# Optimization experiments

Hardware: AMD Instinct MI355X
Metric: run time of the kernel (lower is better)

Reference implementation:

```python
import jax, jax.numpy as jnp
import numpy as np

B, S, P, G, E = 16, 1024, 32, 64, 512
HD = E // 2          # head_dim = 256
SCALE = HD ** -0.5
LAMBDA_INIT = 0.8 - 0.6 * float(np.exp(-0.3 * 0.0))  # depth=0 -> 0.2
EPS = 1e-5


def setup_inputs() -> dict:
    key = jax.random.key(0)
    ks = jax.random.split(key, 12)
    inp = {
        'query': jax.random.normal(ks[0], (B, S, E), jnp.float32),
        'key': jax.random.normal(ks[1], (B, P, G, E), jnp.float32),
        'mask': jax.random.randint(ks[2], (B, S), 0, 2).astype(bool),
        'Wq': jax.random.normal(ks[3], (E, E), jnp.float32) * (E ** -0.5),
        'Wk': jax.random.normal(ks[4], (E, E), jnp.float32) * (E ** -0.5),
        'Wv': jax.random.normal(ks[5], (E, E), jnp.float32) * (E ** -0.5),
        'Wo': jax.random.normal(ks[6], (E, E), jnp.float32) * (E ** -0.5),
        'lq1': jax.random.normal(ks[7], (HD,), jnp.float32) * 0.1,
        'lk1': jax.random.normal(ks[8], (HD,), jnp.float32) * 0.1,
        'lq2': jax.random.normal(ks[9], (HD,), jnp.float32) * 0.1,
        'lk2': jax.random.normal(ks[10], (HD,), jnp.float32) * 0.1,
        'gamma': jnp.ones((E,), jnp.float32),
    }
    return inp


def reference(query, key, mask, Wq, Wk, Wv, Wo, lq1, lk1, lq2, lk2, gamma):
    b, s, e = query.shape
    _, p, g, _ = key.shape
    L = p * g
    key2d = key.reshape(b, L, e)

    Q = (query @ Wq).reshape(b, s, 2, HD).transpose(0, 2, 1, 3) * SCALE  # [B,2,S,hd]
    K = (key2d @ Wk).reshape(b, L, 2, HD).transpose(0, 2, 1, 3)          # [B,2,L,hd]
    V = key2d @ Wv                                                       # [B,L,E]

    scores = jnp.einsum('bhsd,bhld->bhsl', Q, K)                         # [B,2,S,L]
    # masked_fill(~mask, 0.0) with mask broadcast [B,1,S,1]
    scores = jnp.where(mask[:, None, :, None], scores, 0.0)
    attn = jax.nn.softmax(scores, axis=-1)

    lam1 = jnp.exp(jnp.sum(lq1 * lk1))
    lam2 = jnp.exp(jnp.sum(lq2 * lk2))
    lam = lam1 - lam2 + LAMBDA_INIT

    diff = attn[:, 0] - lam * attn[:, 1]                                 # [B,S,L]
    out2d = jnp.einsum('bsl,ble->bse', diff, V)                          # [B,S,E]

    # RMSNorm over last dim with affine gamma
    rms = out2d * jax.lax.rsqrt(jnp.mean(out2d * out2d, axis=-1, keepdims=True) + EPS)
    rms = rms * gamma
    out = (rms * (1.0 - LAMBDA_INIT)) @ Wo                               # [B,S,E]

    return out, diff.reshape(b, s, p, g)
```

## Files before the change

### kernel.cpp

```cpp
#include <hip/hip_runtime.h>
#include <hip/hip_bf16.h>


typedef short short8 __attribute__((ext_vector_type(8)));
typedef __bf16 bf16x8 __attribute__((ext_vector_type(8)));
typedef float f32x4 __attribute__((ext_vector_type(4)));

#define LDS_BYTES 16384
#define OUT0_ELEMS 8388608L

__global__ void probe_kernel(const void* gamma, const void* mask, int* flags)
{
    if (threadIdx.x == 0) {
        unsigned g = *(const unsigned*)gamma;
        flags[0] = (g == 0x3F800000u) ? 1 : 0;
        flags[1] = 0;
    }
    __syncthreads();
    const unsigned* mi = (const unsigned*)mask;
    int bad = 0;
    for (int i = threadIdx.x; i < 4096; i += blockDim.x)
        if (mi[i] > 1u) bad = 1;
    if (bad) atomicOr(&flags[1], 1);
}

__global__ void convert_mask(const void* __restrict__ mask, int* __restrict__ mi,
                             const int* __restrict__ flags)
{
    int i = blockIdx.x * 256 + threadIdx.x;
    if (flags[1]) mi[i] = ((const unsigned char*)mask)[i] ? 1 : 0;
    else          mi[i] = ((const int*)mask)[i] ? 1 : 0;
}

__device__ __forceinline__ float read_elem(const void* p, int i, int isf32)
{
    return isf32 ? ((const float*)p)[i]
                 : __bfloat162float(((const __hip_bfloat16*)p)[i]);
}

__global__ void convert_gamma(const void* __restrict__ gamma, float* __restrict__ g,
                              const int* __restrict__ flags)
{
    int i = blockIdx.x * 256 + threadIdx.x;
    g[i] = read_elem(gamma, i, flags[0]);
}

__global__ void transpose_w(const void* __restrict__ Wq, const void* __restrict__ Wk,
                            const void* __restrict__ Wv, const void* __restrict__ Wo,
                            __hip_bfloat16* __restrict__ dst, const int* __restrict__ flags)
{
    int which = blockIdx.y;
    const void* s = (which == 0) ? Wq : (which == 1) ? Wk : (which == 2) ? Wv : Wo;
    __hip_bfloat16* d = dst + (long)which * 262144;
    int idx = blockIdx.x * 256 + threadIdx.x;
    int k = idx >> 9, n = idx & 511;
    d[n * 512 + k] = __float2bfloat16(read_elem(s, idx, flags[0]));
}

__global__ void lam_kernel(const void* __restrict__ lq1, const void* __restrict__ lk1,
                           const void* __restrict__ lq2, const void* __restrict__ lk2,
                           float* __restrict__ lamp, const int* __restrict__ flags)
{
    int t = threadIdx.x;
    int f = flags[0];
    float s1 = 0.0f, s2 = 0.0f;
#pragma unroll
    for (int j = 0; j < 4; ++j) {
        int idx = t * 4 + j;
        s1 += read_elem(lq1, idx, f) * read_elem(lk1, idx, f);
        s2 += read_elem(lq2, idx, f) * read_elem(lk2, idx, f);
    }
#pragma unroll
    for (int off = 1; off < 64; off <<= 1) {
        s1 += __shfl_xor(s1, off);
        s2 += __shfl_xor(s2, off);
    }
    if (t == 0) *lamp = __expf(s1) - __expf(s2) + 0.2f;
}

__global__ void zero_lst(float* __restrict__ lst)
{
    lst[blockIdx.x * 256 + threadIdx.x] = 0.0f;
}

__device__ __forceinline__ void stage_u(const void* A, long aoff, int lda, int af32,
                                        const __hip_bfloat16* B, int ldb,
                                        int kt, char* smem, int tid)
{
    if (af32) {
#pragma unroll
        for (int j = 0; j < 2; ++j) {
            int chunk = j * 256 + tid;
            const float* g = (const float*)A + aoff + (long)(chunk >> 2) * lda + kt + (chunk & 3) * 8;
            f32x4 x0 = *(const f32x4*)g;
            f32x4 x1 = *(const f32x4*)(g + 4);
            __hip_bfloat16 tmp[8];
#pragma unroll
            for (int t = 0; t < 4; ++t) tmp[t] = __float2bfloat16(x0[t]);
#pragma unroll
            for (int t = 0; t < 4; ++t) tmp[4 + t] = __float2bfloat16(x1[t]);
            *(short8*)(smem + chunk * 16) = *(const short8*)tmp;
        }
    } else {
#pragma unroll
        for (int j = 0; j < 2; ++j) {
            int chunk = j * 256 + tid;
            const __hip_bfloat16* g = (const __hip_bfloat16*)A + aoff
                                    + (long)(chunk >> 2) * lda + kt + (chunk & 3) * 8;
            __builtin_amdgcn_global_load_lds(
                (__attribute__((address_space(1))) void*)g,
                (__attribute__((address_space(3))) void*)(smem + chunk * 16), 16, 0, 0);
        }
    }
#pragma unroll
    for (int j = 0; j < 2; ++j) {
        int chunk = j * 256 + tid;
        const __hip_bfloat16* g = B + (long)(chunk >> 2) * ldb + kt + (chunk & 3) * 8;
        __builtin_amdgcn_global_load_lds(
            (__attribute__((address_space(1))) void*)g,
            (__attribute__((address_space(3))) void*)(smem + 8192 + chunk * 16), 16, 0, 0);
    }
}

__device__ __forceinline__ void mfma_block(char* smem, int tid, f32x4 (&acc)[4][4])
{
    const int lane = tid & 63, wid = tid >> 6;
    const int wm = wid >> 1, wn = wid & 1;
    const int lm = lane & 15, lq = lane >> 4;
    short8 a[4], b[4];
#pragma unroll
    for (int i = 0; i < 4; ++i)
        a[i] = *(const short8*)(smem + (wm * 64 + i * 16 + lm) * 64 + lq * 16);
#pragma unroll
    for (int i = 0; i < 4; ++i)
        b[i] = *(const short8*)(smem + 8192 + (wn * 64 + i * 16 + lm) * 64 + lq * 16);
#pragma unroll
    for (int i = 0; i < 4; ++i)
#pragma unroll
        for (int j = 0; j < 4; ++j)
            acc[i][j] = __builtin_amdgcn_mfma_f32_16x16x32_bf16(
                __builtin_bit_cast(bf16x8, a[i]),
                __builtin_bit_cast(bf16x8, b[j]),
                acc[i][j], 0, 0, 0);
}

__device__ __forceinline__ void zero_acc(f32x4 (&acc)[4][4])
{
#pragma unroll
    for (int i = 0; i < 4; ++i)
#pragma unroll
        for (int j = 0; j < 4; ++j)
#pragma unroll
            for (int r = 0; r < 4; ++r) acc[i][j][r] = 0.0f;
}

__device__ __forceinline__ void tile_gemm_u(const void* A, long aoff, int lda, int af32,
                                            const __hip_bfloat16* B, int ldb, int K,
                                            char* smem, int tid, f32x4 (&acc)[4][4])
{
    zero_acc(acc);
    for (int kt = 0; kt < K; kt += 32) {
        __syncthreads();
        stage_u(A, aoff, lda, af32, B, ldb, kt, smem, tid);
        __syncthreads();
        mfma_block(smem, tid, acc);
    }
}

template <int MODE, int AF>
__launch_bounds__(256, 4)
__global__ void gemm_u(const void* __restrict__ A,
                       const __hip_bfloat16* __restrict__ B,
                       void* __restrict__ C,
                       int K, int lda, int ldb, int ldc,
                       long sA, long sB, long sC, float scale,
                       const int* __restrict__ flags)
{
    __shared__ __align__(16) char smem[LDS_BYTES];
    const int tid = threadIdx.x;
    const int bn = blockIdx.x, bm = blockIdx.y, bz = blockIdx.z;
    const int af32 = AF ? flags[0] : 0;
    const long aoff = (long)bz * sA + (long)bm * 128 * lda;
    const __hip_bfloat16* Bb = B + (long)bz * sB + (long)bn * 128 * ldb;

    f32x4 acc[4][4];
    tile_gemm_u(A, aoff, lda, af32, Bb, ldb, K, smem, tid, acc);

    const int f32o = (MODE == 3) ? flags[0] : 0;
    const int lane = tid & 63, wid = tid >> 6;
    const int wm = wid >> 1, wn = wid & 1;
    const int lm = lane & 15, lq = lane >> 4;
#pragma unroll
    for (int im = 0; im < 4; ++im)
#pragma unroll
        for (int in = 0; in < 4; ++in)
#pragma unroll
            for (int r = 0; r < 4; ++r) {
                int row = bm * 128 + wm * 64 + im * 16 + lq * 4 + r;
                int col = bn * 128 + wn * 64 + in * 16 + lm;
                float v = acc[im][in][r] * scale;
                if (MODE == 0) {
                    ((__hip_bfloat16*)C)[bz * sC + (long)row * ldc + col] = __float2bfloat16(v);
                } else if (MODE == 2) {
                    ((float*)C)[bz * sC + (long)row * ldc + col] = v;
                } else if (MODE == 3) {
                    long idx = bz * sC + (long)row * ldc + col;
                    if (f32o) ((float*)C)[idx] = v;
                    else      ((__hip_bfloat16*)C)[idx] = __float2bfloat16(v);
                } else {
                    int bb = row >> 11, l = row & 2047;
                    ((__hip_bfloat16*)C)[((long)bb * 512 + col) * 2048 + l] = __float2bfloat16(v);
                }
            }
}

__device__ __forceinline__ void score_epilogue(
    f32x4 (&acc)[4][4], char* smem, int tid,
    int nt, int st, int b, int bl, const int* __restrict__ mask,
    float* __restrict__ lstats, __hip_bfloat16* __restrict__ P, int h)
{
    const int lane = tid & 63, wid = tid >> 6;
    const int wm = wid >> 1, wn = wid & 1;
    const int lm = lane & 15, lq = lane >> 4;
    float esum[4][4];
#pragma unroll
    for (int im = 0; im < 4; ++im)
#pragma unroll
        for (int r = 0; r < 4; ++r) {
            int rl = wm * 64 + im * 16 + lq * 4 + r;
            int s  = st * 128 + rl;
            int mv = mask[b * 1024 + s];
            float es = 0.0f;
#pragma unroll
            for (int in = 0; in < 4; ++in) {
                int col = nt * 128 + wn * 64 + in * 16 + lm;
                float sc = mv ? acc[im][in][r] : 0.0f;
                float e  = __expf(sc);
                P[((long)bl * 1024 + s) * 2048 + col] = __float2bfloat16(e);
                float t = e;
                t += __shfl_xor(t, 1);
                t += __shfl_xor(t, 2);
                t += __shfl_xor(t, 4);
                t += __shfl_xor(t, 8);
                es += t;
            }
            esum[im][r] = es;
        }
    __syncthreads();
    float* red = (float*)smem;
    if (lm == 0) {
#pragma unroll
        for (int im = 0; im < 4; ++im)
#pragma unroll
            for (int r = 0; r < 4; ++r)
                red[wn * 128 + wm * 64 + im * 16 + lq * 4 + r] = esum[im][r];
    }
    __syncthreads();
    if (tid < 128)
        atomicAdd(&lstats[((long)(b * 2 + h)) * 1024 + st * 128 + tid],
                  red[tid] + red[128 + tid]);
}

__launch_bounds__(256, 3)
__global__ void score_kernel(const __hip_bfloat16* __restrict__ Q,
                             const __hip_bfloat16* __restrict__ Km,
                             const int* __restrict__ mask,
                             float* __restrict__ lstats,
                             __hip_bfloat16* __restrict__ P0,
                             __hip_bfloat16* __restrict__ P1,
                             int bbase)
{
    __shared__ __align__(16) char smem[LDS_BYTES];
    const int tid = threadIdx.x;
    const int nt = blockIdx.x, st = blockIdx.y, bl = blockIdx.z;
    const int b = bl + bbase;
    const long A0 = ((long)b * 1024 + st * 128) * 512;
    const __hip_bfloat16* B0 = Km + ((long)b * 2048 + nt * 128) * 512;

    f32x4 acc[4][4];
    tile_gemm_u(Q, A0, 512, 0, B0, 512, 256, smem, tid, acc);
    score_epilogue(acc, smem, tid, nt, st, b, bl, mask, lstats, P0, 0);
    tile_gemm_u(Q, A0 + 256, 512, 0, B0 + 256, 512, 256, smem, tid, acc);
    score_epilogue(acc, smem, tid, nt, st, b, bl, mask, lstats, P1, 1);
}

__launch_bounds__(256, 2)
__global__ void dv_wide(const __hip_bfloat16* __restrict__ P0,
                        const __hip_bfloat16* __restrict__ P1,
                        const __hip_bfloat16* __restrict__ Vt,
                        const float* __restrict__ lst,
                        const float* __restrict__ lamp,
                        float* __restrict__ o2d,
                        void* __restrict__ dout,
                        const int* __restrict__ flags)
{
    __shared__ __align__(16) char smem[36864];
    const int tid = threadIdx.x;
    const int bm = blockIdx.x, b = blockIdx.y;
    const float lam = *lamp;

    const int arow = tid >> 2;
    const int acol = (tid & 3) * 8;
    const int srow = bm * 32 + (arow & 31);
    float i0 = 0.0f, i1 = 0.0f;
    if (tid < 128) {
        i0 = 1.0f / lst[((long)(b * 2)) * 1024 + srow];
        i1 = lam  / lst[((long)(b * 2 + 1)) * 1024 + srow];
    }
    const __hip_bfloat16* Bb = Vt + (long)b * (512L * 2048);
    const int f32o = flags[0];
    float* doutF = (float*)dout + OUT0_ELEMS;
    __hip_bfloat16* doutH = (__hip_bfloat16*)dout + OUT0_ELEMS;

    f32x4 acc[2][8];
#pragma unroll
    for (int im = 0; im < 2; ++im)
#pragma unroll
        for (int in = 0; in < 8; ++in)
#pragma unroll
            for (int r = 0; r < 4; ++r) acc[im][in][r] = 0.0f;

    const int lane = tid & 63, wid = tid >> 6;
    const int lm = lane & 15, lq = lane >> 4;

    for (int kt = 0; kt < 2048; kt += 32) {
        __syncthreads();
#pragma unroll
        for (int j = 0; j < 8; ++j) {
            int chunk = j * 256 + tid;
            const __hip_bfloat16* g = Bb + (long)(chunk >> 2) * 2048 + kt + (chunk & 3) * 8;
            __builtin_amdgcn_global_load_lds(
                (__attribute__((address_space(1))) void*)g,
                (__attribute__((address_space(3))) void*)(smem + 4096 + chunk * 16), 16, 0, 0);
        }
        float d[8];
        union { short8 v; __hip_bfloat16 h[8]; } ta;
        if (tid < 128) {
            long off = ((long)b * 1024 + srow) * 2048 + kt + acol;
            union { short8 v; __hip_bfloat16 h[8]; } u0, u1;
            u0.v = *(const short8*)(P0 + off);
            u1.v = *(const short8*)(P1 + off);
#pragma unroll
            for (int t = 0; t < 8; ++t)
                d[t] = __bfloat162float(u0.h[t]) * i0 - __bfloat162float(u1.h[t]) * i1;
#pragma unroll
            for (int t = 0; t < 8; ++t) ta.h[t] = __float2bfloat16(d[t]);
            *(short8*)(smem + (arow & 31) * 64 + (tid & 3) * 16) = ta.v;
        }
        __syncthreads();
        if (tid < 128) {
            long g = ((long)b * 1024 + srow) * 2048 + kt + acol;
            if (f32o) {
                f32x4 v0, v1;
#pragma unroll
                for (int t = 0; t < 4; ++t) { v0[t] = d[t]; v1[t] = d[4 + t]; }
                *(f32x4*)(doutF + g)     = v0;
                *(f32x4*)(doutF + g + 4) = v1;
            } else {
                *(short8*)(doutH + g) = ta.v;
            }
        }
        short8 af[2], bf[8];
#pragma unroll
        for (int im = 0; im < 2; ++im)
            af[im] = *(const short8*)(smem + (im * 16 + lm) * 64 + lq * 16);
#pragma unroll
        for (int in = 0; in < 8; ++in)
            bf[in] = *(const short8*)(smem + 4096 + (wid * 128 + in * 16 + lm) * 64 + lq * 16);
#pragma unroll
        for (int im = 0; im < 2; ++im)
#pragma unroll
            for (int in = 0; in < 8; ++in)
                acc[im][in] = __builtin_amdgcn_mfma_f32_16x16x32_bf16(
                    __builtin_bit_cast(bf16x8, af[im]),
                    __builtin_bit_cast(bf16x8, bf[in]),
                    acc[im][in], 0, 0, 0);
    }

#pragma unroll
    for (int im = 0; im < 2; ++im)
#pragma unroll
        for (int in = 0; in < 8; ++in)
#pragma unroll
            for (int r = 0; r < 4; ++r) {
                int row = bm * 32 + im * 16 + lq * 4 + r;
                int col = wid * 128 + in * 16 + lm;
                o2d[((long)b * 1024 + row) * 512 + col] = acc[im][in][r];
            }
}

__launch_bounds__(256, 3)
__global__ void dv_fused(const __hip_bfloat16* __restrict__ P0,
                         const __hip_bfloat16* __restrict__ P1,
                         const __hip_bfloat16* __restrict__ Vt,
                         const float* __restrict__ lst,
                         const float* __restrict__ lamp,
                         float* __restrict__ o2d,
                         void* __restrict__ dout,
                         int bbase, const int* __restrict__ flags)
{
    __shared__ __align__(16) char smem[LDS_BYTES];
    const int tid = threadIdx.x;
    const int bn = blockIdx.x, bm = blockIdx.y, bz = blockIdx.z;
    const int b = bz + bbase;
    const float lam = *lamp;

    int srow[2]; float i0[2], i1[2];
#pragma unroll
    for (int j = 0; j < 2; ++j) {
        srow[j] = bm * 128 + j * 64 + (tid >> 2);
        i0[j] = 1.0f / lst[((long)(b * 2)) * 1024 + srow[j]];
        i1[j] = lam  / lst[((long)(b * 2 + 1)) * 1024 + srow[j]];
    }

    const __hip_bfloat16* Bb = Vt + (long)b * (512L * 2048) + (long)bn * 128 * 2048;
    const int f32o = flags[0];
    float* doutF = (float*)dout + OUT0_ELEMS;
    __hip_bfloat16* doutH = (__hip_bfloat16*)dout + OUT0_ELEMS;

    f32x4 acc[4][4];
    zero_acc(acc);

    for (int kt = 0; kt < 2048; kt += 32) {
        __syncthreads();
#pragma unroll
        for (int j = 0; j < 2; ++j) {
            int chunk = j * 256 + tid;
            int kc = kt + (chunk & 3) * 8;
            long off = ((long)bz * 1024 + srow[j]) * 2048 + kc;
            union { short8 v; __hip_bfloat16 h[8]; } u0, u1;
            u0.v = *(const short8*)(P0 + off);
            u1.v = *(const short8*)(P1 + off);
            float d[8];
#pragma unroll
            for (int t = 0; t < 8; ++t)
                d[t] = __bfloat162float(u0.h[t]) * i0[j]
                     - __bfloat162float(u1.h[t]) * i1[j];
            __hip_bfloat16 tmp[8];
#pragma unroll
            for (int t = 0; t < 8; ++t) tmp[t] = __float2bfloat16(d[t]);
            *(short8*)(smem + chunk * 16) = *(const short8*)tmp;
            if (bn == 0) {
                long g = ((long)b * 1024 + srow[j]) * 2048 + kc;
                if (f32o) {
                    f32x4 v0, v1;
#pragma unroll
                    for (int t = 0; t < 4; ++t) { v0[t] = d[t]; v1[t] = d[4 + t]; }
                    *(f32x4*)(doutF + g)     = v0;
                    *(f32x4*)(doutF + g + 4) = v1;
                } else {
                    *(short8*)(doutH + g) = *(const short8*)tmp;
                }
            }
        }
#pragma unroll
        for (int j = 0; j < 2; ++j) {
            int chunk = j * 256 + tid;
            const __hip_bfloat16* g = Bb + (long)(chunk >> 2) * 2048 + kt + (chunk & 3) * 8;
            __builtin_amdgcn_global_load_lds(
                (__attribute__((address_space(1))) void*)g,
                (__attribute__((address_space(3))) void*)(smem + 8192 + chunk * 16), 16, 0, 0);
        }
        __syncthreads();
        mfma_block(smem, tid, acc);
    }

    const int lane = tid & 63, wid = tid >> 6;
    const int wm = wid >> 1, wn = wid & 1;
    const int lm = lane & 15, lq = lane >> 4;
#pragma unroll
    for (int im = 0; im < 4; ++im)
#pragma unroll
        for (int in = 0; in < 4; ++in)
#pragma unroll
            for (int r = 0; r < 4; ++r) {
                int row = bm * 128 + wm * 64 + im * 16 + lq * 4 + r;
                int col = bn * 128 + wn * 64 + in * 16 + lm;
                o2d[((long)b * 1024 + row) * 512 + col] = acc[im][in][r];
            }
}

__global__ void finalize_kernel(__hip_bfloat16* P0,
                                const __hip_bfloat16* __restrict__ P1,
                                const float* __restrict__ lstats,
                                const float* __restrict__ lamp,
                                void* dout, int bbase,
                                const int* __restrict__ flags)
{
    const long row = blockIdx.x;
    const int bl = (int)(row >> 10), s = (int)(row & 1023);
    const int b  = bl + bbase;
    const int tid = threadIdx.x;
    const float lam = *lamp;
    const float i0 = 1.0f / lstats[((long)(b * 2)) * 1024 + s];
    const float i1 = lam  / lstats[((long)(b * 2 + 1)) * 1024 + s];
    const long lbase = row * 2048 + (long)tid * 8;

    union { short8 v; __hip_bfloat16 h[8]; } u0, u1, ub;
    u0.v = *(const short8*)(P0 + lbase);
    u1.v = *(const short8*)(P1 + lbase);
    float d[8];
#pragma unroll
    for (int j = 0; j < 8; ++j)
        d[j] = __bfloat162float(u0.h[j]) * i0 - __bfloat162float(u1.h[j]) * i1;

    const long gidx = ((long)b * 1024 + s) * 2048 + (long)tid * 8;
    if (flags[0]) {
        float* outF = (float*)dout + OUT0_ELEMS;
        f32x4 v0, v1;
#pragma unroll
        for (int j = 0; j < 4; ++j) { v0[j] = d[j]; v1[j] = d[4 + j]; }
        *(f32x4*)(outF + gidx)     = v0;
        *(f32x4*)(outF + gidx + 4) = v1;
    } else {
        __hip_bfloat16* outH = (__hip_bfloat16*)dout + OUT0_ELEMS;
        union { short8 v; __hip_bfloat16 h[8]; } uo;
#pragma unroll
        for (int j = 0; j < 8; ++j) uo.h[j] = __float2bfloat16(d[j]);
        *(short8*)(outH + gidx) = uo.v;
    }
#pragma unroll
    for (int j = 0; j < 8; ++j) ub.h[j] = __float2bfloat16(d[j]);
    *(short8*)(P0 + lbase) = ub.v;
}

__global__ void rmsnorm_kernel(const float* __restrict__ X,
                               const float* __restrict__ gamma,
                               __hip_bfloat16* __restrict__ Y)
{
    long row = blockIdx.x;
    int lane = threadIdx.x;
    const float* x = X + row * 512 + lane * 8;
    f32x4 v0 = *(const f32x4*)x;
    f32x4 v1 = *(const f32x4*)(x + 4);
    float ss = v0[0] * v0[0] + v0[1] * v0[1] + v0[2] * v0[2] + v0[3] * v0[3]
             + v1[0] * v1[0] + v1[1] * v1[1] + v1[2] * v1[2] + v1[3] * v1[3];
#pragma unroll
    for (int off = 1; off < 64; off <<= 1) ss += __shfl_xor(ss, off);
    float rinv = rsqrtf(ss * (1.0f / 512.0f) + 1e-5f) * 0.8f;
#pragma unroll
    for (int j = 0; j < 4; ++j)
        Y[row * 512 + lane * 8 + j] = __float2bfloat16(v0[j] * rinv * gamma[lane * 8 + j]);
#pragma unroll
    for (int j = 0; j < 4; ++j)
        Y[row * 512 + lane * 8 + 4 + j] = __float2bfloat16(v1[j] * rinv * gamma[lane * 8 + 4 + j]);
}

extern "C" void kernel_launch(void* const* d_in, const int* in_sizes, int n_in,
                              void* d_out, int out_size, void* d_ws, size_t ws_size,
                              hipStream_t stream)
{
    const void* query = d_in[0];
    const void* key2d = d_in[1];
    const void* maskp = d_in[2];
    const void* Wq    = d_in[3];
    const void* Wk    = d_in[4];
    const void* Wv    = d_in[5];
    const void* Wo    = d_in[6];
    const void* lq1   = d_in[7];
    const void* lk1   = d_in[8];
    const void* lq2   = d_in[9];
    const void* lk2   = d_in[10];
    const void* gamma = d_in[11];

    char* w = (char*)d_ws;
    __hip_bfloat16* WT    = (__hip_bfloat16*)(w);
    __hip_bfloat16* WqT   = WT;
    __hip_bfloat16* WkT   = WT + 262144;
    __hip_bfloat16* WvT   = WT + 524288;
    __hip_bfloat16* WoT   = WT + 786432;
    float*          lamp  = (float*)(w + 2097152);
    int*            flags = (int*)(w + 2097216);
    float*          gammaF= (float*)(w + 2097280);
    int*            maskI = (int*)(w + 2162688);
    __hip_bfloat16* Qb    = (__hip_bfloat16*)(w + 2228224);
    __hip_bfloat16* Kb    = (__hip_bfloat16*)(w + 19005440);
    __hip_bfloat16* Vt    = (__hip_bfloat16*)(w + 52559872);
    float*          lst   = (float*)(w + 86114304);
    float*          o2d   = (float*)(w + 86245376);
    __hip_bfloat16* rmsb  = (__hip_bfloat16*)(w + 119799808);
    __hip_bfloat16* diffBF= (__hip_bfloat16*)(w + 136577024);
    __hip_bfloat16* P1s   = (__hip_bfloat16*)(w + 103022592);

    const bool hugews = ws_size >= 270794752UL;
    const bool bigws  = ws_size >= 203685888UL;

    probe_kernel<<<1, 256, 0, stream>>>(gamma, maskp, flags);
    convert_mask<<<64, 256, 0, stream>>>(maskp, maskI, flags);
    convert_gamma<<<2, 256, 0, stream>>>(gamma, gammaF, flags);
    transpose_w<<<dim3(1024, 4, 1), 256, 0, stream>>>(Wq, Wk, Wv, Wo, WT, flags);
    lam_kernel<<<1, 64, 0, stream>>>(lq1, lk1, lq2, lk2, lamp, flags);
    zero_lst<<<128, 256, 0, stream>>>(lst);

    gemm_u<0, 1><<<dim3(4, 128, 1), 256, 0, stream>>>(query, WqT, Qb,
        512, 512, 512, 512, 0, 0, 0, 0.0625f, flags);
    gemm_u<0, 1><<<dim3(4, 256, 1), 256, 0, stream>>>(key2d, WkT, Kb,
        512, 512, 512, 512, 0, 0, 0, 1.0f, flags);
    gemm_u<1, 1><<<dim3(4, 256, 1), 256, 0, stream>>>(key2d, WvT, Vt,
        512, 512, 512, 0, 0, 0, 0, 1.0f, flags);

    if (hugews) {
        __hip_bfloat16* P0f = diffBF;
        __hip_bfloat16* P1f = diffBF + 33554432L;
        score_kernel<<<dim3(16, 8, 16), 256, 0, stream>>>(Qb, Kb, maskI, lst,
            P0f, P1f, 0);
        dv_wide<<<dim3(32, 16), 256, 0, stream>>>(P0f, P1f, Vt, lst, lamp,
            o2d, d_out, flags);
    } else if (bigws) {
        __hip_bfloat16* P0h = diffBF;
        __hip_bfloat16* P1h = diffBF + 16777216L;
        for (int h = 0; h < 2; ++h) {
            int bb = h * 8;
            score_kernel<<<dim3(16, 8, 8), 256, 0, stream>>>(Qb, Kb, maskI, lst,
                P0h, P1h, bb);
            dv_fused<<<dim3(4, 8, 8), 256, 0, stream>>>(P0h, P1h, Vt, lst, lamp,
                o2d, d_out, bb, flags);
        }
    } else {
        __hip_bfloat16* scratch = (__hip_bfloat16*)d_out;
        for (int h = 0; h < 2; ++h) {
            int bb = h * 8;
            score_kernel<<<dim3(16, 8, 8), 256, 0, stream>>>(Qb, Kb, maskI, lst,
                scratch, P1s, bb);
            finalize_kernel<<<8192, 256, 0, stream>>>(scratch, P1s, lst, lamp,
                d_out, bb, flags);
            gemm_u<2, 0><<<dim3(4, 8, 8), 256, 0, stream>>>(scratch,
                Vt + (long)bb * 512 * 2048, o2d + (long)bb * 1024 * 512,
                2048, 2048, 2048, 512, 1024L * 2048, 512L * 2048, 1024L * 512, 1.0f, flags);
        }
    }

    rmsnorm_kernel<<<16384, 64, 0, stream>>>(o2d, gammaF, rmsb);

    gemm_u<3, 0><<<dim3(4, 128, 1), 256, 0, stream>>>(rmsb, WoT, d_out,
        512, 512, 512, 512, 0, 0, 1024L * 512, 1.0f, flags);
}
```

Baseline: 671.2 us.

## Split-K the diff@V kernel in two, summing partials inside RMSNorm

The wide diff@V kernel gains a second grid dimension that splits the 2048-long reduction into two halves. Each half writes its own fp32 partial output, and the RMSNorm kernel now adds the two partials before normalising. The kernel also prefetches the next P0/P1 chunk into registers, XOR-swizzles the LDS layout to cut bank conflicts, and raises the launch-bounds occupancy target from 2 to 4. The trade-offs are an extra 32 MB partial buffer and a higher workspace threshold for this path, so smaller workspaces fall back to the slower chunked path.

Result: slower. 838.0 us (+24.8%).

```diff
diff --git a/kernel.cpp b/kernel.cpp
--- a/kernel.cpp
+++ b/kernel.cpp
@@ -284,24 +284,26 @@
     score_epilogue(acc, smem, tid, nt, st, b, bl, mask, lstats, P1, 1);
 }
 
-__launch_bounds__(256, 2)
+__launch_bounds__(256, 4)
 __global__ void dv_wide(const __hip_bfloat16* __restrict__ P0,
                         const __hip_bfloat16* __restrict__ P1,
                         const __hip_bfloat16* __restrict__ Vt,
                         const float* __restrict__ lst,
                         const float* __restrict__ lamp,
-                        float* __restrict__ o2d,
+                        float* __restrict__ o2dA,
+                        float* __restrict__ o2dB,
                         void* __restrict__ dout,
                         const int* __restrict__ flags)
 {
     __shared__ __align__(16) char smem[36864];
     const int tid = threadIdx.x;
-    const int bm = blockIdx.x, b = blockIdx.y;
+    const int bm = blockIdx.x, b = blockIdx.y, ks = blockIdx.z;
+    const int k0 = ks * 1024, kend = k0 + 1024;
     const float lam = *lamp;
 
-    const int arow = tid >> 2;
-    const int acol = (tid & 3) * 8;
-    const int srow = bm * 32 + (arow & 31);
+    const int arow = (tid >> 2) & 31;
+    const int ac   = tid & 3;
+    const int srow = bm * 32 + arow;
     float i0 = 0.0f, i1 = 0.0f;
     if (tid < 128) {
         i0 = 1.0f / lst[((long)(b * 2)) * 1024 + srow];
@@ -311,6 +313,7 @@
     const int f32o = flags[0];
     float* doutF = (float*)dout + OUT0_ELEMS;
     __hip_bfloat16* doutH = (__hip_bfloat16*)dout + OUT0_ELEMS;
+    const long arowoff = ((long)b * 1024 + srow) * 2048;
 
     f32x4 acc[2][8];
 #pragma unroll
@@ -323,33 +326,42 @@
     const int lane = tid & 63, wid = tid >> 6;
     const int lm = lane & 15, lq = lane >> 4;
 
-    for (int kt = 0; kt < 2048; kt += 32) {
+    union U8 { short8 v; __hip_bfloat16 h[8]; };
+    U8 c0, c1, n0, n1;
+    if (tid < 128) {
+        c0.v = *(const short8*)(P0 + arowoff + k0 + ac * 8);
+        c1.v = *(const short8*)(P1 + arowoff + k0 + ac * 8);
+    }
+
+    for (int kt = k0; kt < kend; kt += 32) {
         __syncthreads();
 #pragma unroll
         for (int j = 0; j < 8; ++j) {
             int chunk = j * 256 + tid;
-            const __hip_bfloat16* g = Bb + (long)(chunk >> 2) * 2048 + kt + (chunk & 3) * 8;
+            int n = chunk >> 2, c = chunk & 3;
+            int csrc = c ^ (n & 3);
+            const __hip_bfloat16* g = Bb + (long)n * 2048 + kt + csrc * 8;
             __builtin_amdgcn_global_load_lds(
                 (__attribute__((address_space(1))) void*)g,
                 (__attribute__((address_space(3))) void*)(smem + 4096 + chunk * 16), 16, 0, 0);
         }
         float d[8];
-        union { short8 v; __hip_bfloat16 h[8]; } ta;
+        U8 ta;
         if (tid < 128) {
-            long off = ((long)b * 1024 + srow) * 2048 + kt + acol;
-            union { short8 v; __hip_bfloat16 h[8]; } u0, u1;
-            u0.v = *(const short8*)(P0 + off);
-            u1.v = *(const short8*)(P1 + off);
 #pragma unroll
             for (int t = 0; t < 8; ++t)
-                d[t] = __bfloat162float(u0.h[t]) * i0 - __bfloat162float(u1.h[t]) * i1;
+                d[t] = __bfloat162float(c0.h[t]) * i0 - __bfloat162float(c1.h[t]) * i1;
 #pragma unroll
             for (int t = 0; t < 8; ++t) ta.h[t] = __float2bfloat16(d[t]);
-            *(short8*)(smem + (arow & 31) * 64 + (tid & 3) * 16) = ta.v;
+            *(short8*)(smem + arow * 64 + (ac ^ (arow & 3)) * 16) = ta.v;
+            if (kt + 32 < kend) {
+                n0.v = *(const short8*)(P0 + arowoff + kt + 32 + ac * 8);
+                n1.v = *(const short8*)(P1 + arowoff + kt + 32 + ac * 8);
+            }
         }
         __syncthreads();
         if (tid < 128) {
-            long g = ((long)b * 1024 + srow) * 2048 + kt + acol;
+            long g = arowoff + kt + ac * 8;
             if (f32o) {
                 f32x4 v0, v1;
 #pragma unroll
@@ -359,14 +371,19 @@
             } else {
                 *(short8*)(doutH + g) = ta.v;
             }
+            c0 = n0; c1 = n1;
         }
         short8 af[2], bf[8];
 #pragma unroll
-        for (int im = 0; im < 2; ++im)
-            af[im] = *(const short8*)(smem + (im * 16 + lm) * 64 + lq * 16);
-#pragma unroll
-        for (int in = 0; in < 8; ++in)
-            bf[in] = *(const short8*)(smem + 4096 + (wid * 128 + in * 16 + lm) * 64 + lq * 16);
+        for (int im = 0; im < 2; ++im) {
+            int row = im * 16 + lm;
+            af[im] = *(const short8*)(smem + row * 64 + (lq ^ (row & 3)) * 16);
+        }
+#pragma unroll
+        for (int in = 0; in < 8; ++in) {
+            int n = wid * 128 + in * 16 + lm;
+            bf[in] = *(const short8*)(smem + 4096 + n * 64 + (lq ^ (n & 3)) * 16);
+        }
 #pragma unroll
         for (int im = 0; im < 2; ++im)
 #pragma unroll
@@ -377,6 +394,7 @@
                     acc[im][in], 0, 0, 0);
     }
 
+    float* opart = ks ? o2dB : o2dA;
 #pragma unroll
     for (int im = 0; im < 2; ++im)
 #pragma unroll
@@ -385,7 +403,7 @@
             for (int r = 0; r < 4; ++r) {
                 int row = bm * 32 + im * 16 + lq * 4 + r;
                 int col = wid * 128 + in * 16 + lm;
-                o2d[((long)b * 1024 + row) * 512 + col] = acc[im][in][r];
+                opart[((long)b * 1024 + row) * 512 + col] = acc[im][in][r];
             }
 }
 
@@ -524,15 +542,23 @@
     *(short8*)(P0 + lbase) = ub.v;
 }
 
-__global__ void rmsnorm_kernel(const float* __restrict__ X,
+__global__ void rmsnorm_kernel(const float* __restrict__ X0,
+                               const float* __restrict__ X1,
                                const float* __restrict__ gamma,
                                __hip_bfloat16* __restrict__ Y)
 {
     long row = blockIdx.x;
     int lane = threadIdx.x;
-    const float* x = X + row * 512 + lane * 8;
+    const float* x = X0 + row * 512 + lane * 8;
     f32x4 v0 = *(const f32x4*)x;
     f32x4 v1 = *(const f32x4*)(x + 4);
+    if (X1) {
+        const float* y = X1 + row * 512 + lane * 8;
+        f32x4 w0 = *(const f32x4*)y;
+        f32x4 w1 = *(const f32x4*)(y + 4);
+#pragma unroll
+        for (int j = 0; j < 4; ++j) { v0[j] += w0[j]; v1[j] += w1[j]; }
+    }
     float ss = v0[0] * v0[0] + v0[1] * v0[1] + v0[2] * v0[2] + v0[3] * v0[3]
              + v1[0] * v1[0] + v1[1] * v1[1] + v1[2] * v1[2] + v1[3] * v1[3];
 #pragma unroll
@@ -580,9 +606,10 @@
     float*          o2d   = (float*)(w + 86245376);
     __hip_bfloat16* rmsb  = (__hip_bfloat16*)(w + 119799808);
     __hip_bfloat16* diffBF= (__hip_bfloat16*)(w + 136577024);
+    float*          o2dB  = (float*)(w + 270794752);
     __hip_bfloat16* P1s   = (__hip_bfloat16*)(w + 103022592);
 
-    const bool hugews = ws_size >= 270794752UL;
+    const bool hugews = ws_size >= 304349184UL;
     const bool bigws  = ws_size >= 203685888UL;
 
     probe_kernel<<<1, 256, 0, stream>>>(gamma, maskp, flags);
@@ -604,8 +631,9 @@
         __hip_bfloat16* P1f = diffBF + 33554432L;
         score_kernel<<<dim3(16, 8, 16), 256, 0, stream>>>(Qb, Kb, maskI, lst,
             P0f, P1f, 0);
-        dv_wide<<<dim3(32, 16), 256, 0, stream>>>(P0f, P1f, Vt, lst, lamp,
-            o2d, d_out, flags);
+        dv_wide<<<dim3(32, 16, 2), 256, 0, stream>>>(P0f, P1f, Vt, lst, lamp,
+            o2d, o2dB, d_out, flags);
+        rmsnorm_kernel<<<16384, 64, 0, stream>>>(o2d, o2dB, gammaF, rmsb);
     } else if (bigws) {
         __hip_bfloat16* P0h = diffBF;
         __hip_bfloat16* P1h = diffBF + 16777216L;
@@ -616,6 +644,7 @@
             dv_fused<<<dim3(4, 8, 8), 256, 0, stream>>>(P0h, P1h, Vt, lst, lamp,
                 o2d, d_out, bb, flags);
         }
+        rmsnorm_kernel<<<16384, 64, 0, stream>>>(o2d, nullptr, gammaF, rmsb);
     } else {
         __hip_bfloat16* scratch = (__hip_bfloat16*)d_out;
         for (int h = 0; h < 2; ++h) {
@@ -628,9 +657,8 @@
                 Vt + (long)bb * 512 * 2048, o2d + (long)bb * 1024 * 512,
                 2048, 2048, 2048, 512, 1024L * 2048, 512L * 2048, 1024L * 512, 1.0f, flags);
         }
-    }
-
-    rmsnorm_kernel<<<16384, 64, 0, stream>>>(o2d, gammaF, rmsb);
+        rmsnorm_kernel<<<16384, 64, 0, stream>>>(o2d, nullptr, gammaF, rmsb);
+    }
 
     gemm_u<3, 0><<<dim3(4, 128, 1), 256, 0, stream>>>(rmsb, WoT, d_out,
         512, 512, 512, 512, 0, 0, 1024L * 512, 1.0f, flags);
```
